# Optimization experiments

Measured on AMD Instinct MI355X. Metric: run time of the kernel, lower is better.

Reference implementation:

```python
import jax, jax.numpy as jnp
import numpy as np

IN_CH, HID, OUT_CH = 1, 16, 1

def _conv(x, w, b, pad):
    # x: [B,C,H,W], w: [O,I,kh,kw], b: [O]
    y = jax.lax.conv_general_dilated(
        x, w, window_strides=(1, 1), padding=[(pad, pad), (pad, pad)],
        dimension_numbers=('NCHW', 'OIHW', 'NCHW'))
    return y + b[None, :, None, None]

def setup_inputs() -> dict:
    key = jax.random.key(0)
    ks = jax.random.split(key, 8)
    def w_init(k, shape):
        fan_in = shape[1] * shape[2] * shape[3]
        return jax.random.normal(k, shape, dtype=jnp.float32) * (1.0 / np.sqrt(fan_in))
    B, H, W = 32, 256, 256
    return {
        'x': jax.random.normal(ks[0], (B, IN_CH, H, W), dtype=jnp.float32),
        'w_perceive': w_init(ks[1], (HID * 2, IN_CH + HID, 3, 3)),
        'b_perceive': jnp.zeros((HID * 2,), jnp.float32),
        'w_up1': w_init(ks[2], (HID, HID * 2, 1, 1)),
        'b_up1': jnp.zeros((HID,), jnp.float32),
        'w_up2': w_init(ks[3], (HID, HID, 1, 1)),
        'b_up2': jnp.zeros((HID,), jnp.float32),
        'w_tau': w_init(ks[4], (HID, IN_CH + HID * 2, 3, 3)),
        'b_tau_conv': jnp.zeros((HID,), jnp.float32),
        'b_tau': jnp.ones((1, HID, 1, 1), jnp.float32) * 1.5,
        'w_read': w_init(ks[5], (OUT_CH, HID, 1, 1)),
        'b_read': jnp.zeros((OUT_CH,), jnp.float32),
        'n_steps': 10,
    }

def reference(x, w_perceive, b_perceive, w_up1, b_up1, w_up2, b_up2,
              w_tau, b_tau_conv, b_tau, w_read, b_read, n_steps):
    B, _, H, W = x.shape
    state = jnp.zeros((B, HID, H, W), dtype=x.dtype)

    def step(state, _):
        combined = jnp.concatenate([x, state], axis=1)          # [B, in+hid, H, W]
        perception = _conv(combined, w_perceive, b_perceive, 1)  # [B, 2*hid, H, W]
        h1 = jax.nn.relu(_conv(perception, w_up1, b_up1, 0))
        delta = _conv(h1, w_up2, b_up2, 0)                       # [B, hid, H, W]
        tau_input = jnp.concatenate([x, state, delta], axis=1)  # [B, in+2*hid, H, W]
        tau_logit = _conv(tau_input, w_tau, b_tau_conv, 1) + b_tau
        beta = jnp.clip(jax.nn.sigmoid(tau_logit), 0.01, 0.99)
        return beta * state + (1.0 - beta) * delta, None

    state, _ = jax.lax.scan(step, state, None, length=n_steps)
    return jax.nn.sigmoid(_conv(state, w_read, b_read, 0))
```

## Files before the change

### kernel.cpp

```cpp
#include <hip/hip_runtime.h>
#include <hip/hip_bf16.h>
#include <math.h>


#define B_   32
#define H_   256
#define W_   256
#define PIT  40
#define XPP  260

typedef unsigned short ushort_t;
typedef __attribute__((ext_vector_type(8))) short short8;
typedef __attribute__((ext_vector_type(4))) float float4v;

__device__ __forceinline__ unsigned fbits(float f) {
    union { float f; unsigned u; } v; v.f = f; return v.u;
}
__device__ __forceinline__ ushort_t f2bu(float f) {
    return (ushort_t)((fbits(f) + 0x8000u) >> 16);
}
__device__ __forceinline__ unsigned pack2(float lo, float hi) {
    return ((fbits(hi) + 0x8000u) & 0xFFFF0000u) | ((fbits(lo) + 0x8000u) >> 16);
}
__device__ __forceinline__ float bu2f(ushort_t u) {
    union { unsigned i; float f; } v; v.i = ((unsigned)u) << 16; return v.f;
}
__device__ __forceinline__ float lo2f(unsigned u) {
    union { unsigned i; float f; } v; v.i = u << 16; return v.f;
}
__device__ __forceinline__ float hi2f(unsigned u) {
    union { unsigned i; float f; } v; v.i = u & 0xFFFF0000u; return v.f;
}

__global__ void prep(
    const float* __restrict__ wp,
    const float* __restrict__ wu1,
    const float* __restrict__ bu1,
    const float* __restrict__ bp,
    const float* __restrict__ wu2,
    const float* __restrict__ wt,
    const float* __restrict__ btc,
    const float* __restrict__ bt,
    ushort_t* __restrict__ wh1p,
    ushort_t* __restrict__ wu2f,
    ushort_t* __restrict__ wtxf,
    ushort_t* __restrict__ wtn,
    float* __restrict__ scal)
{
    __shared__ float Weff[16 * 153];
    const int tid = threadIdx.x;

    for (int i = tid; i < 16 * 153; i += 256) {
        int j = i / 153, rem = i % 153, c = rem / 9, t = rem % 9;
        float s = 0.f;
        for (int o = 0; o < 32; ++o)
            s += wu1[j * 32 + o] * wp[o * 153 + c * 9 + t];
        Weff[i] = s;
    }
    if (tid < 16) {
        float s = bu1[tid];
        for (int o = 0; o < 32; ++o) s += wu1[tid * 32 + o] * bp[o];
        scal[tid] = s;
    }
    if (tid < 16) scal[32 + tid] = btc[tid] + bt[tid];
    if (tid < 16) scal[48 + tid] = wt[tid * 297 + 8];
    __syncthreads();

    if (tid < 16) scal[16 + tid] = Weff[tid * 153 + 8];

    for (int i = tid; i < 4 * 64 * 8; i += 256) {
        int ii = i >> 9, lane = (i >> 3) & 63, j = i & 7;
        int n = lane & 15, kk = ((lane >> 4) << 3) + j;
        int tap = 2 * ii + (kk >> 4), ch = kk & 15;
        wh1p[i] = f2bu(Weff[n * 153 + (ch + 1) * 9 + tap]);
    }
    for (int i = tid; i < 512; i += 256) {
        int lane = i >> 3, j = i & 7;
        int n = lane & 15, k = ((lane >> 4) << 3) + j;
        float v = 0.f;
        if (k < 16)       v = Weff[n * 153 + (k + 1) * 9 + 8];
        else if (k < 24)  v = Weff[n * 153 + (k - 16)];
        else if (k == 24) v = Weff[n * 153 + 8];
        wh1p[2048 + i] = f2bu(v);
    }
    for (int i = tid; i < 512; i += 256) {
        int lane = i >> 3, j = i & 7;
        int n = lane & 15, k = ((lane >> 4) << 3) + j;
        wu2f[i] = (k < 16) ? f2bu(wu2[n * 16 + k]) : (ushort_t)0;
    }
    for (int i = tid; i < 512; i += 256) {
        int lane = i >> 3, j = i & 7;
        int n = lane & 15, k = ((lane >> 4) << 3) + j;
        wtxf[i] = (k < 8) ? f2bu(wt[n * 297 + k]) : (ushort_t)0;
    }
    for (int i = tid; i < 9 * 64 * 8; i += 256) {
        int t = i / 512, lane = (i / 8) % 64, j = i % 8;
        int n = lane & 15, k = ((lane >> 4) << 3) + j;
        int c = (k < 16) ? (17 + k) : (k - 15);
        wtn[i] = f2bu(wt[n * 297 + c * 9 + t]);
    }
}

__global__ __launch_bounds__(256) void precompute_xp8(
    const float* __restrict__ x,
    ushort_t* __restrict__ xp8)
{
    int idx = blockIdx.x * 256 + threadIdx.x;
    if (idx >= B_ * XPP * XPP) return;
    int b  = idx / (XPP * XPP), rem = idx - b * (XPP * XPP);
    int by = rem / XPP, bx = rem - by * XPP;
    int gy = by - 2, gx = bx - 2;
    const float* xb = x + (size_t)b * 65536;
    short8 v;
#pragma unroll
    for (int t = 0; t < 8; ++t) {
        int yy = gy + t / 3, xx = gx + t % 3;
        bool in = ((unsigned)yy < 256u) & ((unsigned)xx < 256u);
        v[t] = in ? (short)f2bu(xb[yy * 256 + xx]) : (short)0;
    }
    *(short8*)(xp8 + (size_t)idx * 8) = v;
}

__global__ __launch_bounds__(256) void nca_step(
    const ushort_t* __restrict__ stIn,
    ushort_t* __restrict__ stOut,
    const ushort_t* __restrict__ xp8g,
    const ushort_t* __restrict__ wh1p,
    const ushort_t* __restrict__ wu2f,
    const ushort_t* __restrict__ wtxf,
    const ushort_t* __restrict__ wtn,
    const float* __restrict__ scal,
    const float* __restrict__ bu2G,
    const float* __restrict__ wrd,
    const float* __restrict__ brd,
    float* __restrict__ outg,
    int first, int last)
{
    __shared__ ushort_t comb[400 * PIT];

    const int tid  = threadIdx.x;
    const int w    = tid >> 6, lane = tid & 63;
    const int m    = lane & 15, q = lane >> 4;
    const int och  = q * 4;
    const int gx0  = blockIdx.x * 16, gy0 = blockIdx.y * 16;
    const size_t pb = (size_t)blockIdx.z * 65536;
    const size_t xpb = (size_t)blockIdx.z * (XPP * XPP);
    const short8 z8 = {0, 0, 0, 0, 0, 0, 0, 0};
    const float4v z4 = {0.f, 0.f, 0.f, 0.f};

    const bool interior = (blockIdx.x >= 1) & (blockIdx.x <= 14)
                        & (blockIdx.y >= 1) & (blockIdx.y <= 14);

    short8 wh1r[5], wtnr[9];
#pragma unroll
    for (int i = 0; i < 5; ++i) wh1r[i] = *(const short8*)(wh1p + (i * 64 + lane) * 8);
#pragma unroll
    for (int t = 0; t < 9; ++t) wtnr[t] = *(const short8*)(wtn + (t * 64 + lane) * 8);
    const short8 wu2r = *(const short8*)(wu2f + lane * 8);
    const short8 wtxr = *(const short8*)(wtxf + lane * 8);

    float4v beff4, bu24, wr4, tb4, wtx84;
#pragma unroll
    for (int r = 0; r < 4; ++r) {
        beff4[r] = scal[och + r];
        tb4[r]   = scal[32 + och + r];
        wtx84[r] = scal[48 + och + r];
        bu24[r]  = bu2G[och + r];
        wr4[r]   = wrd[och + r];
    }
    const float br = brd[0];

    const int sel = q >> 1;
    int offp[4];
#pragma unroll
    for (int ii = 0; ii < 4; ++ii) {
        int tA = 2 * ii, tB = 2 * ii + 1;
        int oA = ((tA / 3) * 20 + (tA % 3)) * PIT;
        int oB = ((tB / 3) * 20 + (tB % 3)) * PIT;
        offp[ii] = sel ? oB : oA;
    }
    const int chOff = 16 + (q & 1) * 8;
    const int t8off = (2 * 20 + 2) * PIT;
    const int off5  = (q == 0) ? (t8off + 16) : (q == 1) ? (t8off + 24)
                    : (q == 2) ? 32 : (t8off + 32);

    const int bpA = ((m + (q << 5)) & 63) << 2;
    const bool hiq = q >= 2;

    if (interior & (first == 0)) {
        for (int p = tid; p < 400; p += 256) {
            int ry = p / 20, rx = p - ry * 20;
            ushort_t* row = comb + p * PIT;
            const ushort_t* sp = stIn
                + (pb + (size_t)(gy0 + ry - 2) * 256 + (gx0 + rx - 2)) * 16;
            *(short8*)(row + 16) = *(const short8*)(sp);
            *(short8*)(row + 24) = *(const short8*)(sp + 8);
            *(short8*)(row + 32) = *(const short8*)(
                xp8g + (xpb + (size_t)(gy0 + ry) * XPP + (gx0 + rx)) * 8);
        }
    } else {
        for (int p = tid; p < 400; p += 256) {
            int ry = p / 20, rx = p - ry * 20;
            int gy = gy0 + ry - 2, gx = gx0 + rx - 2;
            ushort_t* row = comb + p * PIT;
            bool in = ((unsigned)gy < 256u) & ((unsigned)gx < 256u);
            if (in && !first) {
                const ushort_t* sp = stIn + (pb + gy * 256 + gx) * 16;
                *(short8*)(row + 16) = *(const short8*)(sp);
                *(short8*)(row + 24) = *(const short8*)(sp + 8);
            } else {
                *(short8*)(row + 16) = z8; *(short8*)(row + 24) = z8;
            }
            *(short8*)(row + 32) = *(const short8*)(
                xp8g + (xpb + (size_t)(gy0 + ry) * XPP + (gx0 + rx)) * 8);
        }
    }
    __syncthreads();

    {
        int raw = w * 16 + m;
        int py = raw / 18, px = raw - (raw / 18) * 18;
        for (int i = 0; i < 6; ++i) {
            int g = w + 4 * i; if (g >= 21) break;
            bool vld = raw < 324;
            int pyc = vld ? py : 17, pxc = vld ? px : 17;
            const ushort_t* abase = comb + (pyc * 20 + pxc) * PIT;
            float4v acc = z4;
            __builtin_amdgcn_s_setprio(1);
#pragma unroll
            for (int ii = 0; ii < 4; ++ii) {
                short8 b = *(const short8*)(abase + offp[ii] + chOff);
                acc = __builtin_amdgcn_mfma_f32_16x16x32_bf16(wh1r[ii], b, acc, 0, 0, 0);
            }
            {
                short8 b = *(const short8*)(abase + off5);
                acc = __builtin_amdgcn_mfma_f32_16x16x32_bf16(wh1r[4], b, acc, 0, 0, 0);
            }
            __builtin_amdgcn_s_setprio(0);
            uint2 hv;
            {
                float h0 = fmaxf(acc[0] + beff4[0], 0.f);
                float h1 = fmaxf(acc[1] + beff4[1], 0.f);
                float h2 = fmaxf(acc[2] + beff4[2], 0.f);
                float h3 = fmaxf(acc[3] + beff4[3], 0.f);
                hv.x = pack2(h0, h1); hv.y = pack2(h2, h3);
            }
            int vx0 = __builtin_amdgcn_ds_bpermute(bpA,      (int)hv.x);
            int vy0 = __builtin_amdgcn_ds_bpermute(bpA,      (int)hv.y);
            int vx1 = __builtin_amdgcn_ds_bpermute(bpA + 64, (int)hv.x);
            int vy1 = __builtin_amdgcn_ds_bpermute(bpA + 64, (int)hv.y);
            union { int i4[4]; short8 s8; } bb;
            bb.i4[0] = hiq ? 0 : vx0;  bb.i4[1] = hiq ? 0 : vy0;
            bb.i4[2] = hiq ? 0 : vx1;  bb.i4[3] = hiq ? 0 : vy1;
            float4v d = __builtin_amdgcn_mfma_f32_16x16x32_bf16(wu2r, bb.s8, z4, 0, 0, 0);
            uint2 dv;
            dv.x = pack2(d[0] + bu24[0], d[1] + bu24[1]);
            dv.y = pack2(d[2] + bu24[2], d[3] + bu24[3]);
            if (!interior) {
                int gy = gy0 - 1 + pyc, gx = gx0 - 1 + pxc;
                bool im = ((unsigned)gy < 256u) & ((unsigned)gx < 256u);
                if (!im) { dv.x = 0u; dv.y = 0u; }
            }
            if (vld)
                *(uint2*)(comb + ((pyc + 1) * 20 + (pxc + 1)) * PIT + och) = dv;
            raw += 64; px += 10; py += 3;
            if (px >= 18) { px -= 18; py += 1; }
        }
    }
    __syncthreads();

    {
        const int w4 = w * 4;
#define LDROW(r, dx) (*(const short8*)(comb + (((r) * 20) + (m + 1 + (dx))) * PIT + q * 8))
        short8 Ta0 = LDROW(w4 + 1, 0), Ta1 = LDROW(w4 + 1, 1), Ta2 = LDROW(w4 + 1, 2);
        short8 Tb0 = LDROW(w4 + 2, 0), Tb1 = LDROW(w4 + 2, 1), Tb2 = LDROW(w4 + 2, 2);
#pragma unroll
        for (int i = 0; i < 4; ++i) {
            int g = w4 + i;
            short8 Tc0 = LDROW(g + 3, 0), Tc1 = LDROW(g + 3, 1), Tc2 = LDROW(g + 3, 2);
            short8 bx = *(const short8*)(comb + ((g + 1) * 20 + (m + 1)) * PIT + 32);
            float4v acc = z4;
            __builtin_amdgcn_s_setprio(1);
            acc = __builtin_amdgcn_mfma_f32_16x16x32_bf16(wtnr[0], Ta0, acc, 0, 0, 0);
            acc = __builtin_amdgcn_mfma_f32_16x16x32_bf16(wtnr[1], Ta1, acc, 0, 0, 0);
            acc = __builtin_amdgcn_mfma_f32_16x16x32_bf16(wtnr[2], Ta2, acc, 0, 0, 0);
            acc = __builtin_amdgcn_mfma_f32_16x16x32_bf16(wtnr[3], Tb0, acc, 0, 0, 0);
            acc = __builtin_amdgcn_mfma_f32_16x16x32_bf16(wtnr[4], Tb1, acc, 0, 0, 0);
            acc = __builtin_amdgcn_mfma_f32_16x16x32_bf16(wtnr[5], Tb2, acc, 0, 0, 0);
            acc = __builtin_amdgcn_mfma_f32_16x16x32_bf16(wtnr[6], Tc0, acc, 0, 0, 0);
            acc = __builtin_amdgcn_mfma_f32_16x16x32_bf16(wtnr[7], Tc1, acc, 0, 0, 0);
            acc = __builtin_amdgcn_mfma_f32_16x16x32_bf16(wtnr[8], Tc2, acc, 0, 0, 0);
            acc = __builtin_amdgcn_mfma_f32_16x16x32_bf16(wtxr,   bx,  acc, 0, 0, 0);
            __builtin_amdgcn_s_setprio(0);
            int gy = gy0 + g;
            const size_t pix = pb + gy * 256 + gx0 + m;
            const ushort_t* cpx = comb + ((g + 2) * 20 + (m + 2)) * PIT;
            float x8c = bu2f(comb[((g + 3) * 20 + (m + 3)) * PIT + 32]);
            uint2 su = *(const uint2*)(cpx + 16 + och);
            uint2 du = *(const uint2*)(cpx + och);
            float sold[4] = { lo2f(su.x), hi2f(su.x), lo2f(su.y), hi2f(su.y) };
            float dvv[4]  = { lo2f(du.x), hi2f(du.x), lo2f(du.y), hi2f(du.y) };
            float sn[4];
#pragma unroll
            for (int r = 0; r < 4; ++r) {
                float tl  = acc[r] + tb4[r] + x8c * wtx84[r];
                float e   = __expf(-tl);
                float bta = __builtin_amdgcn_rcpf(1.f + e);
                bta = fminf(fmaxf(bta, 0.01f), 0.99f);
                sn[r] = dvv[r] + bta * (sold[r] - dvv[r]);
            }
            if (!last) {
                uint2 o;
                o.x = pack2(sn[0], sn[1]); o.y = pack2(sn[2], sn[3]);
                *(uint2*)(stOut + pix * 16 + och) = o;
            } else {
                float v = sn[0] * wr4[0] + sn[1] * wr4[1]
                        + sn[2] * wr4[2] + sn[3] * wr4[3];
                v += __shfl_xor(v, 16);
                v += __shfl_xor(v, 32);
                if (q == 0) {
                    float eo = __expf(-(v + br));
                    outg[pix] = __builtin_amdgcn_rcpf(1.f + eo);
                }
            }
            Ta0 = Tb0; Ta1 = Tb1; Ta2 = Tb2;
            Tb0 = Tc0; Tb1 = Tc1; Tb2 = Tc2;
        }
#undef LDROW
    }
}

extern "C" void kernel_launch(void* const* d_in, const int* in_sizes, int n_in,
                              void* d_out, int out_size, void* d_ws, size_t ws_size,
                              hipStream_t stream)
{
    const float* x          = (const float*)d_in[0];
    const float* w_perceive = (const float*)d_in[1];
    const float* b_perceive = (const float*)d_in[2];
    const float* w_up1      = (const float*)d_in[3];
    const float* b_up1      = (const float*)d_in[4];
    const float* w_up2      = (const float*)d_in[5];
    const float* b_up2      = (const float*)d_in[6];
    const float* w_tau      = (const float*)d_in[7];
    const float* b_tau_conv = (const float*)d_in[8];
    const float* b_tau      = (const float*)d_in[9];
    const float* w_read     = (const float*)d_in[10];
    const float* b_read     = (const float*)d_in[11];
    float* out = (float*)d_out;

    const size_t stateElems = (size_t)B_ * H_ * W_ * 16;
    const size_t xp8Elems   = (size_t)B_ * XPP * XPP * 8;

    ushort_t* stA  = (ushort_t*)d_ws;
    ushort_t* stB  = stA + stateElems;
    ushort_t* xp8g = stB + stateElems;
    ushort_t* wh1p = xp8g + xp8Elems;
    ushort_t* wu2f = wh1p + 2560;
    ushort_t* wtxf = wu2f + 512;
    ushort_t* wtn  = wtxf + 512;
    float*    scal = (float*)(wtn + 4608);

    const size_t needBytes = (2 * stateElems + xp8Elems
                              + 2560 + 512 + 512 + 4608) * sizeof(ushort_t)
                           + 64 * sizeof(float);
    if (ws_size < needBytes) return;

    prep<<<dim3(1), dim3(256), 0, stream>>>(
        w_perceive, w_up1, b_up1, b_perceive, w_up2, w_tau,
        b_tau_conv, b_tau, wh1p, wu2f, wtxf, wtn, scal);
    precompute_xp8<<<dim3((B_ * XPP * XPP + 255) / 256), dim3(256), 0, stream>>>(
        x, xp8g);

    ushort_t* cur = stA;
    ushort_t* nxt = stB;
    for (int s = 0; s < 10; ++s) {
        nca_step<<<dim3(16, 16, 32), dim3(256), 0, stream>>>(
            cur, nxt, xp8g, wh1p, wu2f, wtxf, wtn, scal, b_up2,
            w_read, b_read, out, (s == 0) ? 1 : 0, (s == 9) ? 1 : 0);
        ushort_t* t = cur; cur = nxt; nxt = t;
    }
}
```

Baseline: 715.1 us.

## Swizzle block order, use hardware bf16 packing, drop masking, hoist LDS loads

Remaps the flat block index so that consecutive workgroups are spread across batch images and tiles, aiming for better cache and channel locality. bf16 packing now goes through the HIP `__float22bfloat162_rn` intrinsic, which can lower to a native packed conversion instead of integer add/mask sequences. The zero-masking of upper-quad lanes after the bpermute is removed; this relies on the packed up2 weights being zero in those K slots. The LDS loads for state, delta and x are moved ahead of the tau MFMA chain so their latency overlaps with matrix work.

```diff
diff --git a/kernel.cpp b/kernel.cpp
--- a/kernel.cpp
+++ b/kernel.cpp
@@ -20,7 +20,9 @@
     return (ushort_t)((fbits(f) + 0x8000u) >> 16);
 }
 __device__ __forceinline__ unsigned pack2(float lo, float hi) {
-    return ((fbits(hi) + 0x8000u) & 0xFFFF0000u) | ((fbits(lo) + 0x8000u) >> 16);
+    union { __hip_bfloat162 h; unsigned u; } v;
+    v.h = __float22bfloat162_rn(make_float2(lo, hi));
+    return v.u;
 }
 __device__ __forceinline__ float bu2f(ushort_t u) {
     union { unsigned i; float f; } v; v.i = ((unsigned)u) << 16; return v.f;
@@ -142,14 +144,16 @@
     const int w    = tid >> 6, lane = tid & 63;
     const int m    = lane & 15, q = lane >> 4;
     const int och  = q * 4;
-    const int gx0  = blockIdx.x * 16, gy0 = blockIdx.y * 16;
-    const size_t pb = (size_t)blockIdx.z * 65536;
-    const size_t xpb = (size_t)blockIdx.z * (XPP * XPP);
+    const int flat = ((int)blockIdx.z << 8) | ((int)blockIdx.y << 4) | (int)blockIdx.x;
+    const int nf   = ((flat & 7) << 10) | (flat >> 3);
+    const int bxi  = nf & 15, byi = (nf >> 4) & 15, bzi = nf >> 8;
+    const int gx0  = bxi * 16, gy0 = byi * 16;
+    const size_t pb = (size_t)bzi * 65536;
+    const size_t xpb = (size_t)bzi * (XPP * XPP);
     const short8 z8 = {0, 0, 0, 0, 0, 0, 0, 0};
     const float4v z4 = {0.f, 0.f, 0.f, 0.f};
 
-    const bool interior = (blockIdx.x >= 1) & (blockIdx.x <= 14)
-                        & (blockIdx.y >= 1) & (blockIdx.y <= 14);
+    const bool interior = (bxi >= 1) & (bxi <= 14) & (byi >= 1) & (byi <= 14);
 
     short8 wh1r[5], wtnr[9];
 #pragma unroll
@@ -185,7 +189,6 @@
                     : (q == 2) ? 32 : (t8off + 32);
 
     const int bpA = ((m + (q << 5)) & 63) << 2;
-    const bool hiq = q >= 2;
 
     if (interior & (first == 0)) {
         for (int p = tid; p < 400; p += 256) {
@@ -238,20 +241,15 @@
             }
             __builtin_amdgcn_s_setprio(0);
             uint2 hv;
-            {
-                float h0 = fmaxf(acc[0] + beff4[0], 0.f);
-                float h1 = fmaxf(acc[1] + beff4[1], 0.f);
-                float h2 = fmaxf(acc[2] + beff4[2], 0.f);
-                float h3 = fmaxf(acc[3] + beff4[3], 0.f);
-                hv.x = pack2(h0, h1); hv.y = pack2(h2, h3);
-            }
-            int vx0 = __builtin_amdgcn_ds_bpermute(bpA,      (int)hv.x);
-            int vy0 = __builtin_amdgcn_ds_bpermute(bpA,      (int)hv.y);
-            int vx1 = __builtin_amdgcn_ds_bpermute(bpA + 64, (int)hv.x);
-            int vy1 = __builtin_amdgcn_ds_bpermute(bpA + 64, (int)hv.y);
+            hv.x = pack2(fmaxf(acc[0] + beff4[0], 0.f),
+                         fmaxf(acc[1] + beff4[1], 0.f));
+            hv.y = pack2(fmaxf(acc[2] + beff4[2], 0.f),
+                         fmaxf(acc[3] + beff4[3], 0.f));
             union { int i4[4]; short8 s8; } bb;
-            bb.i4[0] = hiq ? 0 : vx0;  bb.i4[1] = hiq ? 0 : vy0;
-            bb.i4[2] = hiq ? 0 : vx1;  bb.i4[3] = hiq ? 0 : vy1;
+            bb.i4[0] = __builtin_amdgcn_ds_bpermute(bpA,      (int)hv.x);
+            bb.i4[1] = __builtin_amdgcn_ds_bpermute(bpA,      (int)hv.y);
+            bb.i4[2] = __builtin_amdgcn_ds_bpermute(bpA + 64, (int)hv.x);
+            bb.i4[3] = __builtin_amdgcn_ds_bpermute(bpA + 64, (int)hv.y);
             float4v d = __builtin_amdgcn_mfma_f32_16x16x32_bf16(wu2r, bb.s8, z4, 0, 0, 0);
             uint2 dv;
             dv.x = pack2(d[0] + bu24[0], d[1] + bu24[1]);
@@ -279,6 +277,10 @@
             int g = w4 + i;
             short8 Tc0 = LDROW(g + 3, 0), Tc1 = LDROW(g + 3, 1), Tc2 = LDROW(g + 3, 2);
             short8 bx = *(const short8*)(comb + ((g + 1) * 20 + (m + 1)) * PIT + 32);
+            const ushort_t* cpx = comb + ((g + 2) * 20 + (m + 2)) * PIT;
+            float x8c = bu2f(comb[((g + 3) * 20 + (m + 3)) * PIT + 32]);
+            uint2 su = *(const uint2*)(cpx + 16 + och);
+            uint2 du = *(const uint2*)(cpx + och);
             float4v acc = z4;
             __builtin_amdgcn_s_setprio(1);
             acc = __builtin_amdgcn_mfma_f32_16x16x32_bf16(wtnr[0], Ta0, acc, 0, 0, 0);
@@ -294,10 +296,6 @@
             __builtin_amdgcn_s_setprio(0);
             int gy = gy0 + g;
             const size_t pix = pb + gy * 256 + gx0 + m;
-            const ushort_t* cpx = comb + ((g + 2) * 20 + (m + 2)) * PIT;
-            float x8c = bu2f(comb[((g + 3) * 20 + (m + 3)) * PIT + 32]);
-            uint2 su = *(const uint2*)(cpx + 16 + och);
-            uint2 du = *(const uint2*)(cpx + och);
             float sold[4] = { lo2f(su.x), hi2f(su.x), lo2f(su.y), hi2f(su.y) };
             float dvv[4]  = { lo2f(du.x), hi2f(du.x), lo2f(du.y), hi2f(du.y) };
             float sn[4];
```

After: 731.0 us. +2.2%, slower.
